# Performance work log

Hardware: AMD Instinct MI355X
Metric: run time of the kernel (lower is better)

## Reference

```python
import jax, jax.numpy as jnp
import numpy as np

NEG_SLOPE = 0.2  # GAT LeakyReLU slope
EPS = 1e-16


def _pagat_conv(x, path_index, W, a, b, heads, out_ch, concat):
    """Path-augmented GAT conv: attention over (head, mid, tail) path triples,
    messages flow tail -> head, softmax-normalized per destination node."""
    N = x.shape[0]
    head, mid, tail = path_index[0], path_index[1], path_index[2]
    h = (x @ W).reshape(N, heads, out_ch)            # [N, H, C]
    # attention logits from all three path positions: [P, H]
    e = (jnp.einsum('phc,hc->ph', h[head], a[0])
         + jnp.einsum('phc,hc->ph', h[mid], a[1])
         + jnp.einsum('phc,hc->ph', h[tail], a[2]))
    e = jax.nn.leaky_relu(e, NEG_SLOPE)
    # segment softmax over paths grouped by destination (head) node
    m = jax.ops.segment_max(e, head, num_segments=N)  # [N, H]
    ex = jnp.exp(e - m[head])
    s = jax.ops.segment_sum(ex, head, num_segments=N)  # [N, H]
    alpha = ex / (s[head] + EPS)                       # [P, H]
    # aggregate tail features weighted by attention
    out = jax.ops.segment_sum(alpha[..., None] * h[tail], head, num_segments=N)  # [N, H, C]
    if concat:
        out = out.reshape(N, heads * out_ch)
    else:
        out = out.mean(axis=1)
    return out + b


def setup_inputs() -> dict:
    key = jax.random.key(0)
    ks = jax.random.split(key, 8)
    N, F_in, H, C, CLS, P = 100000, 500, 8, 16, 16, 1000000
    x = jax.random.normal(ks[0], (N, F_in), dtype=jnp.float32)
    path_index = jax.random.randint(ks[1], (3, P), 0, N, dtype=jnp.int32)
    W1 = jax.random.normal(ks[2], (F_in, H * C), dtype=jnp.float32) * 0.05
    a1 = jax.random.normal(ks[3], (3, H, C), dtype=jnp.float32) * 0.05
    b1 = jnp.zeros((H * C,), dtype=jnp.float32)
    W2 = jax.random.normal(ks[4], (H * C, CLS), dtype=jnp.float32) * 0.05
    a2 = jax.random.normal(ks[5], (3, 1, CLS), dtype=jnp.float32) * 0.05
    b2 = jnp.zeros((CLS,), dtype=jnp.float32)
    return {"x": x, "path_index": path_index, "W1": W1, "a1": a1, "b1": b1,
            "W2": W2, "a2": a2, "b2": b2}


def reference(x, path_index, W1, a1, b1, W2, a2, b2):
    # eval mode: dropout is identity
    h = _pagat_conv(x, path_index, W1, a1, b1, heads=8, out_ch=16, concat=True)
    h = jax.nn.elu(h)
    h = _pagat_conv(h, path_index, W2, a2, b2, heads=1, out_ch=16, concat=False)
    return jax.nn.log_softmax(h, axis=1)
```

## Files before the change

### kernel.cpp

```cpp
#include <hip/hip_runtime.h>
#include <hip/hip_bf16.h>

#define F_IN  500
#define HC    128
#define NHEAD 8
#define CDIM  16
#define NCLS  16
#define KPAD  512

static __device__ __forceinline__ float bf(const __hip_bfloat16 v) {
    return __bfloat162float(v);
}

static __device__ __forceinline__ unsigned int enc_f32(float f) {
    unsigned int u = __float_as_uint(f);
    return (u & 0x80000000u) ? ~u : (u | 0x80000000u);
}
static __device__ __forceinline__ float dec_f32(unsigned int u) {
    return __uint_as_float((u & 0x80000000u) ? (u & 0x7FFFFFFFu) : ~u);
}

typedef __bf16 bf16x8 __attribute__((ext_vector_type(8)));
typedef float f32x4 __attribute__((ext_vector_type(4)));

static __device__ __forceinline__ void gload16(const void* g, void* l) {
    __builtin_amdgcn_global_load_lds(
        (const __attribute__((address_space(1))) void*)g,
        (__attribute__((address_space(3))) void*)l, 16, 0, 0);
}

static __device__ __forceinline__ unsigned ldsoff(const void* p) {
    return (unsigned)(size_t)(const __attribute__((address_space(3))) void*)p;
}

static __device__ __forceinline__ void ds_read_f4(unsigned addr, float4& out) {
    asm volatile("ds_read_b128 %0, %1" : "=v"(out) : "v"(addr) : "memory");
}
static __device__ __forceinline__ void ds_read_bf8(unsigned addr, bf16x8& out) {
    asm volatile("ds_read_b128 %0, %1" : "=v"(out) : "v"(addr) : "memory");
}

__global__ void prep_kernel(const float* __restrict__ W1,
                            __bf16* __restrict__ w1t_hi,
                            __bf16* __restrict__ w1t_lo,
                            int* __restrict__ zp, int nz)
{
    int id = blockIdx.x * 256 + threadIdx.x;
    if (id < HC * KPAD) {
        int c = id >> 9, k = id & 511;
        float v = (k < F_IN) ? W1[k * HC + c] : 0.f;
        __bf16 h = (__bf16)v;
        w1t_hi[id] = h;
        w1t_lo[id] = (__bf16)(v - (float)h);
    }
    if (id < nz) zp[id] = 0;
}

static __device__ __forceinline__ void split8(const float4 a, const float4 b,
                                              bf16x8& hi, bf16x8& lo) {
    float v[8] = {a.x, a.y, a.z, a.w, b.x, b.y, b.z, b.w};
#pragma unroll
    for (int j = 0; j < 8; j++) {
        __bf16 h = (__bf16)v[j];
        hi[j] = h;
        lo[j] = (__bf16)(v[j] - (float)h);
    }
}

__global__ __launch_bounds__(256, 2) void gemm1_v5(
    const float* __restrict__ x,
    const __bf16* __restrict__ w1hi, const __bf16* __restrict__ w1lo,
    const float* __restrict__ zpad,
    __hip_bfloat16* __restrict__ h1, int N)
{
    __shared__ float As[3][64 * 32];
    __shared__ __bf16 BsH[3][128 * 32];
    __shared__ __bf16 BsL[3][128 * 32];

    const int tid = threadIdx.x;
    const int lane = tid & 63, wave = tid >> 6;
    const int m = lane & 15, q = lane >> 4;
    const int wr = wave >> 1, wc = wave & 1;
    const int n0 = blockIdx.x * 64;
    const int woff = wave << 10;

    auto stage = [&](int buf, int t) {
        const int k0 = t * 32;
#pragma unroll
        for (int j = 0; j < 2; ++j) {
            int idx = j * 256 + tid;
            {
                int r = idx >> 3, ps = idx & 7;
                int ls = ps ^ (r & 7);
                int kk = k0 + ls * 4;
                int grow = n0 + r;
                const float* src = (kk < F_IN)
                    ? (x + (size_t)(grow < N ? grow : 0) * F_IN + kk)
                    : zpad;
                gload16(src, (char*)&As[buf][0] + j * 4096 + woff);
            }
            {
                int c = idx >> 2, ps2 = idx & 3;
                int ls2 = ps2 ^ (c & 3);
                gload16(w1hi + c * KPAD + k0 + ls2 * 8, (char*)&BsH[buf][0] + j * 4096 + woff);
                gload16(w1lo + c * KPAD + k0 + ls2 * 8, (char*)&BsL[buf][0] + j * 4096 + woff);
            }
        }
    };

    unsigned abase[3], hbase[3], lbase[3];
#pragma unroll
    for (int i = 0; i < 3; ++i) {
        abase[i] = ldsoff(&As[i][0]);
        hbase[i] = ldsoff(&BsH[i][0]);
        lbase[i] = ldsoff(&BsL[i][0]);
    }
    unsigned aoffs[2][2], boffs[4];
#pragma unroll
    for (int rt = 0; rt < 2; ++rt) {
        int r = wr * 32 + rt * 16 + m, x7 = r & 7;
        aoffs[rt][0] = r * 128 + (((2 * q) ^ x7) << 4);
        aoffs[rt][1] = r * 128 + (((2 * q + 1) ^ x7) << 4);
    }
#pragma unroll
    for (int ct = 0; ct < 4; ++ct) {
        int c = wc * 64 + ct * 16 + m;
        boffs[ct] = c * 64 + ((q ^ (c & 3)) << 4);
    }

    f32x4 acc[2][4];
#pragma unroll
    for (int rt = 0; rt < 2; ++rt)
#pragma unroll
        for (int ct = 0; ct < 4; ++ct) acc[rt][ct] = (f32x4){0.f, 0.f, 0.f, 0.f};

    stage(0, 0);
    stage(1, 1);

#pragma unroll
    for (int t = 0; t < 16; ++t) {
        if (t > 0) __builtin_amdgcn_s_barrier();
        if (t + 2 < 16) stage((t + 2) % 3, t + 2);
        if (t < 14)       asm volatile("s_waitcnt vmcnt(12)" ::: "memory");
        else if (t == 14) asm volatile("s_waitcnt vmcnt(6)" ::: "memory");
        else              asm volatile("s_waitcnt vmcnt(0)" ::: "memory");
        __builtin_amdgcn_s_barrier();

        const int cur = t % 3;
        float4 fa[2][2];
        ds_read_f4(abase[cur] + aoffs[0][0], fa[0][0]);
        ds_read_f4(abase[cur] + aoffs[0][1], fa[0][1]);
        ds_read_f4(abase[cur] + aoffs[1][0], fa[1][0]);
        ds_read_f4(abase[cur] + aoffs[1][1], fa[1][1]);
        bf16x8 bh[4], bl[4];
#pragma unroll
        for (int ct = 0; ct < 4; ++ct) {
            ds_read_bf8(hbase[cur] + boffs[ct], bh[ct]);
            ds_read_bf8(lbase[cur] + boffs[ct], bl[ct]);
        }
        asm volatile("s_waitcnt lgkmcnt(0)" ::: "memory");
        __builtin_amdgcn_sched_barrier(0);

        bf16x8 ah[2], al[2];
        split8(fa[0][0], fa[0][1], ah[0], al[0]);
        split8(fa[1][0], fa[1][1], ah[1], al[1]);

        __builtin_amdgcn_s_setprio(1);
#pragma unroll
        for (int rt = 0; rt < 2; ++rt)
#pragma unroll
            for (int ct = 0; ct < 4; ++ct) {
                acc[rt][ct] = __builtin_amdgcn_mfma_f32_16x16x32_bf16(ah[rt], bh[ct], acc[rt][ct], 0, 0, 0);
                acc[rt][ct] = __builtin_amdgcn_mfma_f32_16x16x32_bf16(ah[rt], bl[ct], acc[rt][ct], 0, 0, 0);
                acc[rt][ct] = __builtin_amdgcn_mfma_f32_16x16x32_bf16(al[rt], bh[ct], acc[rt][ct], 0, 0, 0);
            }
        __builtin_amdgcn_s_setprio(0);
    }

#pragma unroll
    for (int rt = 0; rt < 2; ++rt) {
        int rbase = n0 + wr * 32 + rt * 16 + q * 4;
#pragma unroll
        for (int ct = 0; ct < 4; ++ct) {
            int col = wc * 64 + ct * 16 + m;
#pragma unroll
            for (int r = 0; r < 4; ++r) {
                int row = rbase + r;
                if (row < N)
                    h1[(size_t)row * HC + col] = __float2bfloat16(acc[rt][ct][r]);
            }
        }
    }
}

__global__ void dots1_kernel(const __hip_bfloat16* __restrict__ h1,
                             const float* __restrict__ a1,
                             float* __restrict__ d1,
                             unsigned int* __restrict__ gmax, int N)
{
    __shared__ unsigned int sm[16];
    if (threadIdx.x < 16) sm[threadIdx.x] = 0;
    __syncthreads();
    int id = blockIdx.x * blockDim.x + threadIdx.x;
    if (id < N * NHEAD) {
        int n = id >> 3, h = id & 7;
        const __hip_bfloat16* hp = h1 + (size_t)n * HC + h * CDIM;
        float s0 = 0.f, s1 = 0.f, s2 = 0.f;
#pragma unroll
        for (int c = 0; c < CDIM; c++) {
            float v = bf(hp[c]);
            s0 += v * a1[(0 * NHEAD + h) * CDIM + c];
            s1 += v * a1[(1 * NHEAD + h) * CDIM + c];
            s2 += v * a1[(2 * NHEAD + h) * CDIM + c];
        }
        d1[id] = s0;
        d1[N * NHEAD + id] = s1;
        d1[2 * N * NHEAD + id] = s2;
        atomicMax(&sm[h], enc_f32(s1));
        atomicMax(&sm[8 + h], enc_f32(s2));
    }
    __syncthreads();
    if (threadIdx.x < 16) atomicMax(&gmax[threadIdx.x], sm[threadIdx.x]);
}

__global__ void hist_kernel(const int* __restrict__ pidx, int* __restrict__ deg, int P) {
    int p = blockIdx.x * blockDim.x + threadIdx.x;
    if (p < P) atomicAdd(deg + pidx[p], 1);
}

__global__ void scan1_kernel(const int* __restrict__ deg, int* __restrict__ start,
                             int* __restrict__ bsum, int N) {
    __shared__ int sh[256];
    int i = blockIdx.x * 256 + threadIdx.x;
    int v = (i < N) ? deg[i] : 0;
    sh[threadIdx.x] = v;
    __syncthreads();
#pragma unroll
    for (int off = 1; off < 256; off <<= 1) {
        int x = (threadIdx.x >= off) ? sh[threadIdx.x - off] : 0;
        __syncthreads();
        sh[threadIdx.x] += x;
        __syncthreads();
    }
    if (i < N) start[i] = sh[threadIdx.x] - v;
    if (threadIdx.x == 255) bsum[blockIdx.x] = sh[255];
}

__global__ void scan2_kernel(int* __restrict__ bsum, int nb) {
    __shared__ int sh[512];
    int v = (threadIdx.x < nb) ? bsum[threadIdx.x] : 0;
    sh[threadIdx.x] = v;
    __syncthreads();
#pragma unroll
    for (int off = 1; off < 512; off <<= 1) {
        int x = (threadIdx.x >= off) ? sh[threadIdx.x - off] : 0;
        __syncthreads();
        sh[threadIdx.x] += x;
        __syncthreads();
    }
    if (threadIdx.x < nb) bsum[threadIdx.x] = sh[threadIdx.x] - v;
}

__global__ void scan3_kernel(int* __restrict__ start, const int* __restrict__ bsum, int N) {
    int i = blockIdx.x * 256 + threadIdx.x;
    if (i < N) start[i] += bsum[blockIdx.x];
}

__global__ void scatter_kernel(const int* __restrict__ pidx,
                               const int* __restrict__ start,
                               int* __restrict__ cursor,
                               int* __restrict__ csr, int P) {
    int p = blockIdx.x * blockDim.x + threadIdx.x;
    if (p >= P) return;
    int hd = pidx[p];
    int pos = atomicAdd(cursor + hd, 1);
    csr[start[hd] + pos] = p;
}

__global__ __launch_bounds__(256) void attn1_csr_kernel(
    const int* __restrict__ csr, const int* __restrict__ start,
    const int* __restrict__ deg, const int* __restrict__ pidx,
    const float* __restrict__ d1, const __hip_bfloat16* __restrict__ h1,
    const float* __restrict__ b1, const unsigned int* __restrict__ gmax,
    float* __restrict__ elu_out, int N, int P)
{
    int node = blockIdx.x * 4 + (threadIdx.x >> 6);
    if (node >= N) return;
    int lane = threadIdx.x & 63;
    int h = lane >> 3;
    int s0 = start[node], dg = deg[node];
    const float* d1m = d1 + (size_t)N * NHEAD;
    const float* d1t = d1 + (size_t)2 * N * NHEAD;
    const float dh = d1[node * NHEAD + h];
    float zub = dh + dec_f32(gmax[h]) + dec_f32(gmax[8 + h]);
    const float mxub = zub > 0.f ? zub : 0.2f * zub;

    float acc0 = 0.f, acc1 = 0.f, den = 0.f;
    for (int k0 = 0; k0 < dg; k0 += 8) {
        int kk = k0 + (lane & 7);
        bool valid = kk < dg;
        int p = csr[s0 + (valid ? kk : dg - 1)];
        int mid = pidx[P + p], tl = pidx[2 * P + p];
        float z = dh + d1m[mid * NHEAD + h] + d1t[tl * NHEAD + h];
        float e = z > 0.f ? z : 0.2f * z;
        float ex = valid ? __expf(e - mxub) : 0.f;
        den += ex;
        int kmax = dg - k0; if (kmax > 8) kmax = 8;
        for (int dk = 0; dk < kmax; dk++) {
            int tl_b = __shfl(tl, dk, 8);
            float ex_b = __shfl(ex, dk, 8);
            __hip_bfloat162 v = *(const __hip_bfloat162*)(h1 + (size_t)tl_b * HC + 2 * lane);
            acc0 += ex_b * bf(v.x);
            acc1 += ex_b * bf(v.y);
        }
    }
#pragma unroll
    for (int w = 1; w < 8; w <<= 1) den += __shfl_xor(den, w, 8);

    float inv = 1.f / (den + 1e-16f);
    int j0 = 2 * lane;
    float v0 = acc0 * inv + b1[j0];
    float v1 = acc1 * inv + b1[j0 + 1];
    v0 = v0 > 0.f ? v0 : __expf(v0) - 1.f;
    v1 = v1 > 0.f ? v1 : __expf(v1) - 1.f;
    *(float2*)(elu_out + (size_t)node * HC + j0) = make_float2(v0, v1);
}

__global__ __launch_bounds__(256) void layer2_kernel(
    const float* __restrict__ elu, const float* __restrict__ W2,
    const float* __restrict__ a2,
    float* __restrict__ h2, float* __restrict__ d2,
    unsigned int* __restrict__ gmax2, int N)
{
    __shared__ float rows[16][HC + 1];
    __shared__ float h2s[16][NCLS + 1];
    __shared__ unsigned int smax[2];
    const int n0 = blockIdx.x * 16;
    const int tid = threadIdx.x;
    if (tid < 2) smax[tid] = 0;
    for (int idx = tid; idx < 16 * HC; idx += 256) {
        int r = idx >> 7, c = idx & 127;
        rows[r][c] = (n0 + r < N) ? elu[(size_t)(n0 + r) * HC + c] : 0.f;
    }
    __syncthreads();
    int ln = tid >> 4, c = tid & 15;
    float acc = 0.f;
#pragma unroll 8
    for (int j = 0; j < HC; j++) acc += rows[ln][j] * W2[j * NCLS + c];
    h2s[ln][c] = acc;
    if (n0 + ln < N) h2[(size_t)(n0 + ln) * NCLS + c] = acc;
    __syncthreads();
    if (tid < 48) {
        int l = tid / 3, j = tid - l * 3;
        if (n0 + l < N) {
            float s = 0.f;
#pragma unroll
            for (int cc = 0; cc < NCLS; cc++) s += h2s[l][cc] * a2[j * NCLS + cc];
            d2[j * N + n0 + l] = s;
            if (j) atomicMax(&smax[j - 1], enc_f32(s));
        }
    }
    __syncthreads();
    if (tid < 2) atomicMax(&gmax2[tid], smax[tid]);
}

__global__ __launch_bounds__(256) void attn2_csr_kernel(
    const int* __restrict__ csr, const int* __restrict__ start,
    const int* __restrict__ deg, const int* __restrict__ pidx,
    const float* __restrict__ d2, const float* __restrict__ h2,
    const float* __restrict__ b2, const unsigned int* __restrict__ gmax2,
    float* __restrict__ out, int N, int P)
{
    int node = blockIdx.x * 16 + (threadIdx.x >> 4);
    if (node >= N) return;
    int c = threadIdx.x & 15;
    int s0 = start[node], dg = deg[node];
    const float dh = d2[node];
    const float* d2m = d2 + N;
    const float* d2t = d2 + 2 * N;
    float zub = dh + dec_f32(gmax2[0]) + dec_f32(gmax2[1]);
    const float mxub = zub > 0.f ? zub : 0.2f * zub;

    float acc = 0.f, den = 0.f;
    for (int k0 = 0; k0 < dg; k0 += 16) {
        int kk = k0 + c;
        bool valid = kk < dg;
        int p = csr[s0 + (valid ? kk : dg - 1)];
        int mid = pidx[P + p], tl = pidx[2 * P + p];
        float z = dh + d2m[mid] + d2t[tl];
        float e = z > 0.f ? z : 0.2f * z;
        float ex = valid ? __expf(e - mxub) : 0.f;
        den += ex;
        int kmax = dg - k0; if (kmax > 16) kmax = 16;
        for (int dk = 0; dk < kmax; dk++) {
            int tl_b = __shfl(tl, dk, 16);
            float ex_b = __shfl(ex, dk, 16);
            acc += ex_b * h2[(size_t)tl_b * NCLS + c];
        }
    }
#pragma unroll
    for (int w = 1; w < 16; w <<= 1) den += __shfl_xor(den, w, 16);

    float o = acc / (den + 1e-16f) + b2[c];
    float m2 = o;
#pragma unroll
    for (int w = 1; w < 16; w <<= 1) m2 = fmaxf(m2, __shfl_xor(m2, w, 16));
    float ex = __expf(o - m2), sm = ex;
#pragma unroll
    for (int w = 1; w < 16; w <<= 1) sm += __shfl_xor(sm, w, 16);
    float r = o - m2 - __logf(sm);
    out[(size_t)node * NCLS + c] = r;
}

extern "C" void kernel_launch(void* const* d_in, const int* in_sizes, int n_in,
                              void* d_out, int out_size, void* d_ws, size_t ws_size,
                              hipStream_t stream)
{
    const float* x  = (const float*)d_in[0];
    const int*   pi = (const int*)d_in[1];
    const float* W1 = (const float*)d_in[2];
    const float* a1 = (const float*)d_in[3];
    const float* b1 = (const float*)d_in[4];
    const float* W2 = (const float*)d_in[5];
    const float* a2 = (const float*)d_in[6];
    const float* b2 = (const float*)d_in[7];

    const int N = in_sizes[0] / F_IN;
    const int P = in_sizes[1] / 3;

    float* ws = (float*)d_ws;
    size_t off_h1     = 0;
    size_t off_d1     = (size_t)64 * N;
    size_t off_elu    = (size_t)88 * N;
    size_t off_h2     = (size_t)216 * N;
    size_t off_d2     = (size_t)232 * N;
    size_t off_deg    = (size_t)235 * N;
    size_t off_start  = (size_t)236 * N;
    size_t off_cursor = (size_t)237 * N;
    size_t off_gmax   = (size_t)238 * N;
    size_t off_zpad   = (size_t)238 * N + 32;
    size_t off_bsum   = (size_t)238 * N + 96;
    size_t off_csr    = (size_t)238 * N + 96 + 1024;
    size_t off_w1th   = off_csr + P;
    size_t off_w1tl   = off_w1th + 32768;

    __hip_bfloat16* h1 = (__hip_bfloat16*)(ws + off_h1);
    float* d1   = ws + off_d1;
    float* elu  = ws + off_elu;
    float* h2   = ws + off_h2;
    float* d2   = ws + off_d2;
    int* deg    = (int*)(ws + off_deg);
    int* start  = (int*)(ws + off_start);
    int* cursor = (int*)(ws + off_cursor);
    unsigned int* gmax  = (unsigned int*)(ws + off_gmax);
    unsigned int* gmax2 = (unsigned int*)(ws + off_gmax) + 16;
    float* zpad = ws + off_zpad;
    int* bsum   = (int*)(ws + off_bsum);
    int* csr    = (int*)(ws + off_csr);
    __bf16* w1t_hi = (__bf16*)(ws + off_w1th);
    __bf16* w1t_lo = (__bf16*)(ws + off_w1tl);

    const int BLK = 256;
    const int nb = (N + 255) / 256;
    const int nz = 3 * N + 96;

    prep_kernel<<<(nz + 255) / 256, 256, 0, stream>>>(W1, w1t_hi, w1t_lo, deg, nz);
    gemm1_v5<<<(N + 63) / 64, 256, 0, stream>>>(x, w1t_hi, w1t_lo, zpad, h1, N);
    dots1_kernel<<<(N * NHEAD + BLK - 1) / BLK, BLK, 0, stream>>>(h1, a1, d1, gmax, N);
    hist_kernel<<<(P + BLK - 1) / BLK, BLK, 0, stream>>>(pi, deg, P);
    scan1_kernel<<<nb, 256, 0, stream>>>(deg, start, bsum, N);
    scan2_kernel<<<1, 512, 0, stream>>>(bsum, nb);
    scan3_kernel<<<nb, 256, 0, stream>>>(start, bsum, N);
    scatter_kernel<<<(P + BLK - 1) / BLK, BLK, 0, stream>>>(pi, start, cursor, csr, P);
    attn1_csr_kernel<<<(N + 3) / 4, 256, 0, stream>>>(csr, start, deg, pi, d1, h1, b1, gmax, elu, N, P);
    layer2_kernel<<<(N + 15) / 16, 256, 0, stream>>>(elu, W2, a2, h2, d2, gmax2, N);
    attn2_csr_kernel<<<(N + 15) / 16, 256, 0, stream>>>(csr, start, deg, pi, d2, h2, b2, gmax2,
                                                        (float*)d_out, N, P);
}
```

Baseline: 727.9 us.

## Load GEMM1 B operands directly from global in MFMA-fragment layout, deepen A pipeline

```diff
diff --git a/kernel.cpp b/kernel.cpp
--- a/kernel.cpp
+++ b/kernel.cpp
@@ -36,8 +36,13 @@
 static __device__ __forceinline__ void ds_read_f4(unsigned addr, float4& out) {
     asm volatile("ds_read_b128 %0, %1" : "=v"(out) : "v"(addr) : "memory");
 }
-static __device__ __forceinline__ void ds_read_bf8(unsigned addr, bf16x8& out) {
-    asm volatile("ds_read_b128 %0, %1" : "=v"(out) : "v"(addr) : "memory");
+
+template<int OFF>
+static __device__ __forceinline__ bf16x8 gld_b(const __bf16* p) {
+    bf16x8 o;
+    asm volatile("global_load_dwordx4 %0, %1, off offset:%2"
+                 : "=v"(o) : "v"(p), "i"(OFF) : "memory");
+    return o;
 }
 
 __global__ void prep_kernel(const float* __restrict__ W1,
@@ -45,15 +50,18 @@
                             __bf16* __restrict__ w1t_lo,
                             int* __restrict__ zp, int nz)
 {
-    int id = blockIdx.x * 256 + threadIdx.x;
-    if (id < HC * KPAD) {
-        int c = id >> 9, k = id & 511;
+    int e = blockIdx.x * 256 + threadIdx.x;
+    if (e < HC * KPAD) {
+        int j = e & 7, lane = (e >> 3) & 63, ct = (e >> 9) & 3;
+        int t = (e >> 11) & 15, wc = (e >> 15) & 1;
+        int c = wc * 64 + ct * 16 + (lane & 15);
+        int k = t * 32 + (lane >> 4) * 8 + j;
         float v = (k < F_IN) ? W1[k * HC + c] : 0.f;
         __bf16 h = (__bf16)v;
-        w1t_hi[id] = h;
-        w1t_lo[id] = (__bf16)(v - (float)h);
-    }
-    if (id < nz) zp[id] = 0;
+        w1t_hi[e] = h;
+        w1t_lo[e] = (__bf16)(v - (float)h);
+    }
+    if (e < nz) zp[e] = 0;
 }
 
 static __device__ __forceinline__ void split8(const float4 a, const float4 b,
@@ -67,15 +75,13 @@
     }
 }
 
-__global__ __launch_bounds__(256, 2) void gemm1_v5(
+__global__ __launch_bounds__(256, 2) void gemm1_v6(
     const float* __restrict__ x,
     const __bf16* __restrict__ w1hi, const __bf16* __restrict__ w1lo,
     const float* __restrict__ zpad,
     __hip_bfloat16* __restrict__ h1, int N)
 {
-    __shared__ float As[3][64 * 32];
-    __shared__ __bf16 BsH[3][128 * 32];
-    __shared__ __bf16 BsL[3][128 * 32];
+    __shared__ float As[4][64 * 32];
 
     const int tid = threadIdx.x;
     const int lane = tid & 63, wave = tid >> 6;
@@ -89,82 +95,55 @@
 #pragma unroll
         for (int j = 0; j < 2; ++j) {
             int idx = j * 256 + tid;
-            {
-                int r = idx >> 3, ps = idx & 7;
-                int ls = ps ^ (r & 7);
-                int kk = k0 + ls * 4;
-                int grow = n0 + r;
-                const float* src = (kk < F_IN)
-                    ? (x + (size_t)(grow < N ? grow : 0) * F_IN + kk)
-                    : zpad;
-                gload16(src, (char*)&As[buf][0] + j * 4096 + woff);
-            }
-            {
-                int c = idx >> 2, ps2 = idx & 3;
-                int ls2 = ps2 ^ (c & 3);
-                gload16(w1hi + c * KPAD + k0 + ls2 * 8, (char*)&BsH[buf][0] + j * 4096 + woff);
-                gload16(w1lo + c * KPAD + k0 + ls2 * 8, (char*)&BsL[buf][0] + j * 4096 + woff);
-            }
+            int r = idx >> 3, ps = idx & 7;
+            int ls = ps ^ (r & 7);
+            int kk = k0 + ls * 4;
+            int grow = n0 + r;
+            const float* src = (kk < F_IN)
+                ? (x + (size_t)(grow < N ? grow : 0) * F_IN + kk)
+                : zpad;
+            gload16(src, (char*)&As[buf][0] + j * 4096 + woff);
         }
     };
 
-    unsigned abase[3], hbase[3], lbase[3];
-#pragma unroll
-    for (int i = 0; i < 3; ++i) {
-        abase[i] = ldsoff(&As[i][0]);
-        hbase[i] = ldsoff(&BsH[i][0]);
-        lbase[i] = ldsoff(&BsL[i][0]);
-    }
-    unsigned aoffs[2][2], boffs[4];
+    const __bf16* bh_base = w1hi + (size_t)wc * 32768 + (size_t)lane * 8;
+    const __bf16* bl_base = w1lo + (size_t)wc * 32768 + (size_t)lane * 8;
+
+    auto loadB = [&](bf16x8 (&bh)[4], bf16x8 (&bl)[4], int t) {
+        const __bf16* ph = bh_base + (size_t)t * 2048;
+        const __bf16* pl = bl_base + (size_t)t * 2048;
+        bh[0] = gld_b<0>(ph);    bh[1] = gld_b<1024>(ph);
+        bh[2] = gld_b<2048>(ph); bh[3] = gld_b<3072>(ph);
+        bl[0] = gld_b<0>(pl);    bl[1] = gld_b<1024>(pl);
+        bl[2] = gld_b<2048>(pl); bl[3] = gld_b<3072>(pl);
+    };
+
+    unsigned abase[4];
+#pragma unroll
+    for (int i = 0; i < 4; ++i) abase[i] = ldsoff(&As[i][0]);
+    unsigned aoffs[2][2];
 #pragma unroll
     for (int rt = 0; rt < 2; ++rt) {
         int r = wr * 32 + rt * 16 + m, x7 = r & 7;
         aoffs[rt][0] = r * 128 + (((2 * q) ^ x7) << 4);
         aoffs[rt][1] = r * 128 + (((2 * q + 1) ^ x7) << 4);
     }
-#pragma unroll
-    for (int ct = 0; ct < 4; ++ct) {
-        int c = wc * 64 + ct * 16 + m;
-        boffs[ct] = c * 64 + ((q ^ (c & 3)) << 4);
-    }
 
     f32x4 acc[2][4];
 #pragma unroll
     for (int rt = 0; rt < 2; ++rt)
 #pragma unroll
         for (int ct = 0; ct < 4; ++ct) acc[rt][ct] = (f32x4){0.f, 0.f, 0.f, 0.f};
+
+    bf16x8 bhA[4], blA[4], bhB[4], blB[4];
 
     stage(0, 0);
     stage(1, 1);
-
-#pragma unroll
-    for (int t = 0; t < 16; ++t) {
-        if (t > 0) __builtin_amdgcn_s_barrier();
-        if (t + 2 < 16) stage((t + 2) % 3, t + 2);
-        if (t < 14)       asm volatile("s_waitcnt vmcnt(12)" ::: "memory");
-        else if (t == 14) asm volatile("s_waitcnt vmcnt(6)" ::: "memory");
-        else              asm volatile("s_waitcnt vmcnt(0)" ::: "memory");
-        __builtin_amdgcn_s_barrier();
-
-        const int cur = t % 3;
-        float4 fa[2][2];
-        ds_read_f4(abase[cur] + aoffs[0][0], fa[0][0]);
-        ds_read_f4(abase[cur] + aoffs[0][1], fa[0][1]);
-        ds_read_f4(abase[cur] + aoffs[1][0], fa[1][0]);
-        ds_read_f4(abase[cur] + aoffs[1][1], fa[1][1]);
-        bf16x8 bh[4], bl[4];
-#pragma unroll
-        for (int ct = 0; ct < 4; ++ct) {
-            ds_read_bf8(hbase[cur] + boffs[ct], bh[ct]);
-            ds_read_bf8(lbase[cur] + boffs[ct], bl[ct]);
-        }
-        asm volatile("s_waitcnt lgkmcnt(0)" ::: "memory");
-        __builtin_amdgcn_sched_barrier(0);
-
-        bf16x8 ah[2], al[2];
-        split8(fa[0][0], fa[0][1], ah[0], al[0]);
-        split8(fa[1][0], fa[1][1], ah[1], al[1]);
-
+    loadB(bhA, blA, 0);
+    stage(2, 2);
+
+    auto compute = [&](bf16x8 (&bh)[4], bf16x8 (&bl)[4],
+                       bf16x8 (&ah)[2], bf16x8 (&al)[2]) {
         __builtin_amdgcn_s_setprio(1);
 #pragma unroll
         for (int rt = 0; rt < 2; ++rt)
@@ -175,6 +154,38 @@
                 acc[rt][ct] = __builtin_amdgcn_mfma_f32_16x16x32_bf16(al[rt], bh[ct], acc[rt][ct], 0, 0, 0);
             }
         __builtin_amdgcn_s_setprio(0);
+    };
+
+#pragma unroll
+    for (int t = 0; t < 16; ++t) {
+        if (t > 0) __builtin_amdgcn_s_barrier();
+        if (t + 1 < 16) {
+            if ((t & 1) == 0) loadB(bhB, blB, t + 1);
+            else              loadB(bhA, blA, t + 1);
+        }
+        if (t + 3 < 16) stage((t + 3) & 3, t + 3);
+
+        if (t <= 12)      asm volatile("s_waitcnt vmcnt(12)" ::: "memory");
+        else if (t == 13) asm volatile("s_waitcnt vmcnt(10)" ::: "memory");
+        else if (t == 14) asm volatile("s_waitcnt vmcnt(8)" ::: "memory");
+        else              asm volatile("s_waitcnt vmcnt(0)" ::: "memory");
+        __builtin_amdgcn_s_barrier();
+
+        const int cur = t & 3;
+        float4 fa[2][2];
+        ds_read_f4(abase[cur] + aoffs[0][0], fa[0][0]);
+        ds_read_f4(abase[cur] + aoffs[0][1], fa[0][1]);
+        ds_read_f4(abase[cur] + aoffs[1][0], fa[1][0]);
+        ds_read_f4(abase[cur] + aoffs[1][1], fa[1][1]);
+        asm volatile("s_waitcnt lgkmcnt(0)" ::: "memory");
+        __builtin_amdgcn_sched_barrier(0);
+
+        bf16x8 ah[2], al[2];
+        split8(fa[0][0], fa[0][1], ah[0], al[0]);
+        split8(fa[1][0], fa[1][1], ah[1], al[1]);
+
+        if ((t & 1) == 0) compute(bhA, blA, ah, al);
+        else              compute(bhB, blB, ah, al);
     }
 
 #pragma unroll
@@ -205,10 +216,12 @@
     if (id < N * NHEAD) {
         int n = id >> 3, h = id & 7;
         const __hip_bfloat16* hp = h1 + (size_t)n * HC + h * CDIM;
+        bf16x8 v0 = *(const bf16x8*)hp;
+        bf16x8 v1 = *(const bf16x8*)(hp + 8);
         float s0 = 0.f, s1 = 0.f, s2 = 0.f;
 #pragma unroll
         for (int c = 0; c < CDIM; c++) {
-            float v = bf(hp[c]);
+            float v = (c < 8) ? (float)v0[c & 7] : (float)v1[c & 7];
             s0 += v * a1[(0 * NHEAD + h) * CDIM + c];
             s1 += v * a1[(1 * NHEAD + h) * CDIM + c];
             s2 += v * a1[(2 * NHEAD + h) * CDIM + c];
@@ -463,9 +476,10 @@
     const int BLK = 256;
     const int nb = (N + 255) / 256;
     const int nz = 3 * N + 96;
-
-    prep_kernel<<<(nz + 255) / 256, 256, 0, stream>>>(W1, w1t_hi, w1t_lo, deg, nz);
-    gemm1_v5<<<(N + 63) / 64, 256, 0, stream>>>(x, w1t_hi, w1t_lo, zpad, h1, N);
+    const int nprep = (HC * KPAD > nz ? HC * KPAD : nz);
+
+    prep_kernel<<<(nprep + 255) / 256, 256, 0, stream>>>(W1, w1t_hi, w1t_lo, deg, nz);
+    gemm1_v6<<<(N + 63) / 64, 256, 0, stream>>>(x, w1t_hi, w1t_lo, zpad, h1, N);
     dots1_kernel<<<(N * NHEAD + BLK - 1) / BLK, BLK, 0, stream>>>(h1, a1, d1, gmax, N);
     hist_kernel<<<(P + BLK - 1) / BLK, BLK, 0, stream>>>(pi, deg, P);
     scan1_kernel<<<nb, 256, 0, stream>>>(deg, start, bsum, N);
```

New measurement: 725.0 us. About the same (-0.4%).
